# Kernel optimization log

Hardware: AMD Instinct MI355X
Metric: run time of the kernel (lower is better)

Reference implementation:

```python
import jax, jax.numpy as jnp
import numpy as np

D = 1024  # input_size == hidden_size (required by the module's math)
B = 32768

def _linear_params(key, out_dim, in_dim):
    kw, kb = jax.random.split(key)
    bound = 1.0 / np.sqrt(in_dim)
    W = jax.random.uniform(kw, (out_dim, in_dim), jnp.float32, -bound, bound)
    b = jax.random.uniform(kb, (out_dim,), jnp.float32, -bound, bound)
    return W, b

def setup_inputs() -> dict:
    key = jax.random.key(0)
    ks = jax.random.split(key, 8)
    inp = {
        "input": jax.random.normal(ks[0], (B, D), jnp.float32),
        "hidden": jax.random.normal(ks[1], (B, D), jnp.float32),
    }
    names = ["ir", "hr", "iz", "hz", "in_", "hn"]
    for name, k in zip(names, ks[2:]):
        W, b = _linear_params(k, D, D)
        inp[f"W_{name}"] = W
        inp[f"b_{name}"] = b
    return inp

def reference(input, hidden, W_ir, b_ir, W_hr, b_hr, W_iz, b_iz, W_hz, b_hz, W_in_, b_in_, W_hn, b_hn):
    # Fuse the three input-side projections and three hidden-side projections
    # into two GEMMs each mathematically identical to six separate Linears.
    lin = lambda x, W, b: x @ W.T + b
    r_t = jax.nn.sigmoid(lin(input, W_ir, b_ir) + lin(hidden, W_hr, b_hr))
    z_t = jax.nn.sigmoid(lin(input, W_iz, b_iz) + lin(hidden, W_hz, b_hz))
    n_t = jnp.tanh(lin(input, W_in_, b_in_) + r_t * lin(hidden, W_hn, b_hn))
    h_t = (1.0 - z_t) * n_t + z_t * hidden
    return (h_t, h_t)
```

## Files before the change

### kernel.cpp

```cpp
#include <hip/hip_runtime.h>
#include <stdint.h>

#define DD 1024
#define BATCH 32768

typedef unsigned short u16;
typedef __attribute__((ext_vector_type(8))) __bf16 bf16x8;
typedef __attribute__((ext_vector_type(4))) float f32x4;
typedef __attribute__((ext_vector_type(4))) unsigned int u32x4;

__device__ __forceinline__ u16 f2bf(float x) {
  unsigned int u = __builtin_bit_cast(unsigned int, x);
  u = u + 0x7FFFu + ((u >> 16) & 1u);
  return (u16)(u >> 16);
}

__global__ void cvt_all(const float4* __restrict__ in0, const float4* __restrict__ in1,
                        const float4* __restrict__ w0, const float4* __restrict__ w1,
                        const float4* __restrict__ w2, const float4* __restrict__ w3,
                        const float4* __restrict__ w4, const float4* __restrict__ w5,
                        ushort4* __restrict__ o0, ushort4* __restrict__ o1,
                        ushort4* __restrict__ ow) {
  int b = blockIdx.x;
  const float4* s; ushort4* d; int rel;
  if (b < 2048)      { s = in0; d = o0; rel = b; }
  else if (b < 4096) { s = in1; d = o1; rel = b - 2048; }
  else {
    int t = b - 4096; int g = t >> 6; rel = t & 63;
    s = (g == 0) ? w0 : (g == 1) ? w1 : (g == 2) ? w2 : (g == 3) ? w3 : (g == 4) ? w4 : w5;
    d = ow + (size_t)g * 262144;
  }
  int i0 = rel * 4096 + threadIdx.x;
#pragma unroll
  for (int j = 0; j < 16; ++j) {
    int i = i0 + j * 256;
    float4 v = s[i];
    ushort4 o;
    o.x = f2bf(v.x); o.y = f2bf(v.y); o.z = f2bf(v.z); o.w = f2bf(v.w);
    d[i] = o;
  }
}

#define ABUF(b) ((b) * 16384)
#define WBUF(b) (32768 + (b) * 12288)

__device__ __forceinline__ bf16x8 ld8(const u16* p) {
  u32x4 v = *reinterpret_cast<const u32x4*>(p);
  return __builtin_bit_cast(bf16x8, v);
}

__device__ __forceinline__ f32x4 mfma16(bf16x8 a, bf16x8 b, f32x4 c) {
  return __builtin_amdgcn_mfma_f32_16x16x32_bf16(a, b, c, 0, 0, 0);
}

__device__ __forceinline__ void stage_one(const u16* src, const u16* dst) {
  __builtin_amdgcn_global_load_lds(
      (const __attribute__((address_space(1))) void*)src,
      (__attribute__((address_space(3))) void*)dst, 16, 0, 0);
}

__global__ __launch_bounds__(512, 2) void gru_fused(
    const u16* __restrict__ ain, const u16* __restrict__ ah,
    const u16* __restrict__ wall, const float* __restrict__ hidf,
    const float* __restrict__ b_ir, const float* __restrict__ b_hr,
    const float* __restrict__ b_iz, const float* __restrict__ b_hz,
    const float* __restrict__ b_in, const float* __restrict__ b_hn,
    float* __restrict__ out) {
  __shared__ __align__(16) u16 lds[69632];

  int bid = blockIdx.x;
  int x = bid & 7;
  int s = bid >> 3;
  int mb = (x << 4) | (s >> 4);
  int nb = s & 15;

  int tid = threadIdx.x;
  int wid = tid >> 6;
  int lane = tid & 63;
  int r15 = lane & 15;
  int kb = lane >> 4;
  int wm = wid >> 1;
  int wn = wid & 1;

  const f32x4 zero = {0.f, 0.f, 0.f, 0.f};
  f32x4 acc_r[4][2], acc_z[4][2], acc_n[4][2], acc_hn[4][2];
#pragma unroll
  for (int i = 0; i < 4; ++i)
#pragma unroll
    for (int j = 0; j < 2; ++j) {
      acc_r[i][j] = zero; acc_z[i][j] = zero;
      acc_n[i][j] = zero; acc_hn[i][j] = zero;
    }

  int lrow = lane >> 2;
  unsigned koff = (unsigned)((((lane & 3) ^ ((lane >> 3) & 3))) << 3);
  const u16* ain_r = ain + (unsigned)(mb * 256 + lrow) * DD + koff;
  const u16* ah_r  = ah  + (unsigned)(mb * 256 + lrow) * DD + koff;
  const u16* w_r   = wall + (unsigned)(nb * 64 + lrow) * DD + koff;
  int sub = wid & 3;
  int g0 = wid >> 2;
  const u16* wsrc = w_r + (unsigned)(sub * 16) * DD;

  auto stageA = [&](int kt1) {
    unsigned kc = (unsigned)(kt1 << 5);
    int base = ABUF(kt1 & 1);
    stage_one(ain_r + (unsigned)(wid * 16) * DD + kc,       &lds[base + wid * 512]);
    stage_one(ain_r + (unsigned)((wid + 8) * 16) * DD + kc, &lds[base + (wid + 8) * 512]);
    stage_one(ah_r  + (unsigned)(wid * 16) * DD + kc,       &lds[base + 8192 + wid * 512]);
    stage_one(ah_r  + (unsigned)((wid + 8) * 16) * DD + kc, &lds[base + 8192 + (wid + 8) * 512]);
  };
  auto stageW = [&](int kt2, int wb) {
    unsigned kc = (unsigned)(kt2 << 5);
    int base = WBUF(wb);
    stage_one(wsrc + ((unsigned)g0 << 20) + kc,       &lds[base + g0 * 2048 + sub * 512]);
    stage_one(wsrc + ((unsigned)(g0 + 2) << 20) + kc, &lds[base + (g0 + 2) * 2048 + sub * 512]);
    stage_one(wsrc + ((unsigned)(g0 + 4) << 20) + kc, &lds[base + (g0 + 4) * 2048 + sub * 512]);
  };

  int slsw = ((r15 >> 1) & 3);
  int slx = (kb ^ slsw) << 3;

  bf16x8 afi[4], afh[4], bw[6];

  stageA(0); stageW(0, 0); stageA(1); stageW(1, 1);

  int wcur = 0;
  int wnx2 = 2;
  for (int kt = 0; kt < 32; ++kt) {
    if (kt == 0) {
      asm volatile("s_waitcnt vmcnt(7)" ::: "memory");
    } else if (kt == 31) {
      asm volatile("s_waitcnt vmcnt(0)" ::: "memory");
    } else {
      asm volatile("s_waitcnt vmcnt(3)" ::: "memory");
    }
    __builtin_amdgcn_s_barrier();
    __builtin_amdgcn_sched_barrier(0);

    const u16* BA = &lds[ABUF(kt & 1)];
    const u16* BW = &lds[WBUF(wcur)];

#pragma unroll
    for (int i = 0; i < 4; ++i) {
      int Rm = (wm << 6) + (i << 4) + r15;
      afi[i] = ld8(BA + Rm * 32 + slx);
      afh[i] = ld8(BA + 8192 + Rm * 32 + slx);
    }
    {
      int Rn = (wn << 5) + r15;
      const u16* W0 = BW + Rn * 32 + slx;
#pragma unroll
      for (int g = 0; g < 6; ++g) bw[g] = ld8(W0 + g * 2048);
    }
    asm volatile("s_waitcnt lgkmcnt(0)" ::: "memory");
    __builtin_amdgcn_sched_barrier(0);
    if (kt >= 1 && kt < 31) stageA(kt + 1);
    __builtin_amdgcn_s_setprio(1);
#pragma unroll
    for (int i = 0; i < 4; ++i) {
      acc_r[i][0]  = mfma16(afi[i], bw[0], acc_r[i][0]);
      acc_r[i][0]  = mfma16(afh[i], bw[1], acc_r[i][0]);
      acc_z[i][0]  = mfma16(afi[i], bw[2], acc_z[i][0]);
      acc_z[i][0]  = mfma16(afh[i], bw[3], acc_z[i][0]);
      acc_n[i][0]  = mfma16(afi[i], bw[4], acc_n[i][0]);
      acc_hn[i][0] = mfma16(afh[i], bw[5], acc_hn[i][0]);
    }
    __builtin_amdgcn_s_setprio(0);
    __builtin_amdgcn_s_barrier();
    __builtin_amdgcn_sched_barrier(0);

    {
      int Rn = (wn << 5) + 16 + r15;
      const u16* W0 = BW + Rn * 32 + slx;
#pragma unroll
      for (int g = 0; g < 6; ++g) bw[g] = ld8(W0 + g * 2048);
    }
    asm volatile("s_waitcnt lgkmcnt(0)" ::: "memory");
    __builtin_amdgcn_sched_barrier(0);
    if (kt < 30) stageW(kt + 2, wnx2);
    __builtin_amdgcn_s_setprio(1);
#pragma unroll
    for (int i = 0; i < 4; ++i) {
      acc_r[i][1]  = mfma16(afi[i], bw[0], acc_r[i][1]);
      acc_r[i][1]  = mfma16(afh[i], bw[1], acc_r[i][1]);
      acc_z[i][1]  = mfma16(afi[i], bw[2], acc_z[i][1]);
      acc_z[i][1]  = mfma16(afh[i], bw[3], acc_z[i][1]);
      acc_n[i][1]  = mfma16(afi[i], bw[4], acc_n[i][1]);
      acc_hn[i][1] = mfma16(afh[i], bw[5], acc_hn[i][1]);
    }
    __builtin_amdgcn_s_setprio(0);
    wcur = (wcur == 2) ? 0 : wcur + 1;
    wnx2 = (wnx2 == 2) ? 0 : wnx2 + 1;
  }

#pragma unroll
  for (int jf = 0; jf < 2; ++jf) {
    int col = (nb << 6) + (wn << 5) + (jf << 4) + r15;
    float brc = b_ir[col] + b_hr[col];
    float bzc = b_iz[col] + b_hz[col];
    float bnc = b_in[col];
    float bhc = b_hn[col];
#pragma unroll
    for (int i = 0; i < 4; ++i) {
      int row0 = (mb << 8) + (wm << 6) + (i << 4) + (kb << 2);
#pragma unroll
      for (int q = 0; q < 4; ++q) {
        int row = row0 + q;
        float vr = acc_r[i][jf][q] + brc;
        float vz = acc_z[i][jf][q] + bzc;
        float vn = acc_n[i][jf][q] + bnc;
        float vh = acc_hn[i][jf][q] + bhc;
        float rg = __builtin_amdgcn_rcpf(1.f + __expf(-vr));
        float zg = __builtin_amdgcn_rcpf(1.f + __expf(-vz));
        float pre = vn + rg * vh;
        float ax = fabsf(pre);
        float e2 = __expf(-2.f * ax);
        float th = copysignf((1.f - e2) * __builtin_amdgcn_rcpf(1.f + e2), pre);
        float hp = hidf[((size_t)row << 10) + col];
        float h = (1.f - zg) * th + zg * hp;
        size_t o = ((size_t)row << 10) + col;
        out[o] = h;
        out[o + (size_t)BATCH * DD] = h;
      }
    }
  }
}

extern "C" void kernel_launch(void* const* d_in, const int* in_sizes, int n_in,
                              void* d_out, int out_size, void* d_ws, size_t ws_size,
                              hipStream_t stream) {
  (void)in_sizes; (void)n_in; (void)out_size; (void)ws_size;
  const float* inp = (const float*)d_in[0];
  const float* hid = (const float*)d_in[1];
  u16* ws_in  = (u16*)d_ws;
  u16* ws_hid = ws_in + (size_t)BATCH * DD;
  u16* ws_w   = ws_hid + (size_t)BATCH * DD;

  hipLaunchKernelGGL(cvt_all, dim3(4480), dim3(256), 0, stream,
                     (const float4*)inp, (const float4*)hid,
                     (const float4*)d_in[2], (const float4*)d_in[4],
                     (const float4*)d_in[6], (const float4*)d_in[8],
                     (const float4*)d_in[10], (const float4*)d_in[12],
                     (ushort4*)ws_in, (ushort4*)ws_hid, (ushort4*)ws_w);

  hipLaunchKernelGGL(gru_fused, dim3(2048), dim3(512), 0, stream,
                     ws_in, ws_hid, ws_w, hid,
                     (const float*)d_in[3], (const float*)d_in[5],
                     (const float*)d_in[7], (const float*)d_in[9],
                     (const float*)d_in[11], (const float*)d_in[13],
                     (float*)d_out);
}
```

Baseline: 582.3 us.

## Split GEMM main loop into four phases with staggered A staging

The per-k-tile loop now runs four phases instead of two. Each phase loads three W fragments (not six) and then runs a smaller MFMA burst. The A-tile global-to-LDS staging is split into input and hidden halves and issued in different phases, and the prologue no longer prefetches the second A tile. The aim is to interleave LDS reads, global staging and MFMA work more finely and to cut fragment register pressure, at the cost of an extra barrier and lgkmcnt wait per phase.

Result: no change. 577.9 us (-0.8%).

```diff
diff --git a/kernel.cpp b/kernel.cpp
--- a/kernel.cpp
+++ b/kernel.cpp
@@ -101,13 +101,17 @@
   int g0 = wid >> 2;
   const u16* wsrc = w_r + (unsigned)(sub * 16) * DD;
 
-  auto stageA = [&](int kt1) {
+  auto stageAin = [&](int kt1) {
     unsigned kc = (unsigned)(kt1 << 5);
     int base = ABUF(kt1 & 1);
     stage_one(ain_r + (unsigned)(wid * 16) * DD + kc,       &lds[base + wid * 512]);
     stage_one(ain_r + (unsigned)((wid + 8) * 16) * DD + kc, &lds[base + (wid + 8) * 512]);
-    stage_one(ah_r  + (unsigned)(wid * 16) * DD + kc,       &lds[base + 8192 + wid * 512]);
-    stage_one(ah_r  + (unsigned)((wid + 8) * 16) * DD + kc, &lds[base + 8192 + (wid + 8) * 512]);
+  };
+  auto stageAh = [&](int kt1) {
+    unsigned kc = (unsigned)(kt1 << 5);
+    int base = ABUF(kt1 & 1);
+    stage_one(ah_r + (unsigned)(wid * 16) * DD + kc,       &lds[base + 8192 + wid * 512]);
+    stage_one(ah_r + (unsigned)((wid + 8) * 16) * DD + kc, &lds[base + 8192 + (wid + 8) * 512]);
   };
   auto stageW = [&](int kt2, int wb) {
     unsigned kc = (unsigned)(kt2 << 5);
@@ -117,19 +121,16 @@
     stage_one(wsrc + ((unsigned)(g0 + 4) << 20) + kc, &lds[base + (g0 + 4) * 2048 + sub * 512]);
   };
 
-  int slsw = ((r15 >> 1) & 3);
-  int slx = (kb ^ slsw) << 3;
-
-  bf16x8 afi[4], afh[4], bw[6];
-
-  stageA(0); stageW(0, 0); stageA(1); stageW(1, 1);
+  int slx = ((kb ^ ((r15 >> 1) & 3))) << 3;
+
+  bf16x8 afi[4], afh[4], bwA[3], bwB[3];
+
+  stageAin(0); stageAh(0); stageW(0, 0); stageW(1, 1);
 
   int wcur = 0;
   int wnx2 = 2;
   for (int kt = 0; kt < 32; ++kt) {
-    if (kt == 0) {
-      asm volatile("s_waitcnt vmcnt(7)" ::: "memory");
-    } else if (kt == 31) {
+    if (kt == 31) {
       asm volatile("s_waitcnt vmcnt(0)" ::: "memory");
     } else {
       asm volatile("s_waitcnt vmcnt(3)" ::: "memory");
@@ -139,6 +140,8 @@
 
     const u16* BA = &lds[ABUF(kt & 1)];
     const u16* BW = &lds[WBUF(wcur)];
+    const u16* W0 = BW + ((wn << 5) + r15) * 32 + slx;
+    const u16* W1 = BW + ((wn << 5) + 16 + r15) * 32 + slx;
 
 #pragma unroll
     for (int i = 0; i < 4; ++i) {
@@ -146,49 +149,69 @@
       afi[i] = ld8(BA + Rm * 32 + slx);
       afh[i] = ld8(BA + 8192 + Rm * 32 + slx);
     }
-    {
-      int Rn = (wn << 5) + r15;
-      const u16* W0 = BW + Rn * 32 + slx;
-#pragma unroll
-      for (int g = 0; g < 6; ++g) bw[g] = ld8(W0 + g * 2048);
-    }
-    asm volatile("s_waitcnt lgkmcnt(0)" ::: "memory");
-    __builtin_amdgcn_sched_barrier(0);
-    if (kt >= 1 && kt < 31) stageA(kt + 1);
-    __builtin_amdgcn_s_setprio(1);
-#pragma unroll
-    for (int i = 0; i < 4; ++i) {
-      acc_r[i][0]  = mfma16(afi[i], bw[0], acc_r[i][0]);
-      acc_r[i][0]  = mfma16(afh[i], bw[1], acc_r[i][0]);
-      acc_z[i][0]  = mfma16(afi[i], bw[2], acc_z[i][0]);
-      acc_z[i][0]  = mfma16(afh[i], bw[3], acc_z[i][0]);
-      acc_n[i][0]  = mfma16(afi[i], bw[4], acc_n[i][0]);
-      acc_hn[i][0] = mfma16(afh[i], bw[5], acc_hn[i][0]);
-    }
-    __builtin_amdgcn_s_setprio(0);
-    __builtin_amdgcn_s_barrier();
-    __builtin_amdgcn_sched_barrier(0);
-
-    {
-      int Rn = (wn << 5) + 16 + r15;
-      const u16* W0 = BW + Rn * 32 + slx;
-#pragma unroll
-      for (int g = 0; g < 6; ++g) bw[g] = ld8(W0 + g * 2048);
-    }
-    asm volatile("s_waitcnt lgkmcnt(0)" ::: "memory");
-    __builtin_amdgcn_sched_barrier(0);
+    bwA[0] = ld8(W0);
+    bwA[1] = ld8(W0 + 2048);
+    bwA[2] = ld8(W0 + 4096);
+    if (kt < 31) stageAin(kt + 1);
+    __builtin_amdgcn_s_barrier();
+    asm volatile("s_waitcnt lgkmcnt(0)" ::: "memory");
+    __builtin_amdgcn_sched_barrier(0);
+    __builtin_amdgcn_s_setprio(1);
+#pragma unroll
+    for (int i = 0; i < 4; ++i) {
+      acc_r[i][0] = mfma16(afi[i], bwA[0], acc_r[i][0]);
+      acc_r[i][0] = mfma16(afh[i], bwA[1], acc_r[i][0]);
+      acc_z[i][0] = mfma16(afi[i], bwA[2], acc_z[i][0]);
+    }
+    __builtin_amdgcn_s_setprio(0);
+
+    bwB[0] = ld8(W0 + 6144);
+    bwB[1] = ld8(W0 + 8192);
+    bwB[2] = ld8(W0 + 10240);
+    if (kt < 31) stageAh(kt + 1);
+    __builtin_amdgcn_s_barrier();
+    asm volatile("s_waitcnt lgkmcnt(0)" ::: "memory");
+    __builtin_amdgcn_sched_barrier(0);
+    __builtin_amdgcn_s_setprio(1);
+#pragma unroll
+    for (int i = 0; i < 4; ++i) {
+      acc_z[i][0]  = mfma16(afh[i], bwB[0], acc_z[i][0]);
+      acc_n[i][0]  = mfma16(afi[i], bwB[1], acc_n[i][0]);
+      acc_hn[i][0] = mfma16(afh[i], bwB[2], acc_hn[i][0]);
+    }
+    __builtin_amdgcn_s_setprio(0);
+
+    bwA[0] = ld8(W1);
+    bwA[1] = ld8(W1 + 2048);
+    bwA[2] = ld8(W1 + 4096);
     if (kt < 30) stageW(kt + 2, wnx2);
-    __builtin_amdgcn_s_setprio(1);
-#pragma unroll
-    for (int i = 0; i < 4; ++i) {
-      acc_r[i][1]  = mfma16(afi[i], bw[0], acc_r[i][1]);
-      acc_r[i][1]  = mfma16(afh[i], bw[1], acc_r[i][1]);
-      acc_z[i][1]  = mfma16(afi[i], bw[2], acc_z[i][1]);
-      acc_z[i][1]  = mfma16(afh[i], bw[3], acc_z[i][1]);
-      acc_n[i][1]  = mfma16(afi[i], bw[4], acc_n[i][1]);
-      acc_hn[i][1] = mfma16(afh[i], bw[5], acc_hn[i][1]);
-    }
-    __builtin_amdgcn_s_setprio(0);
+    __builtin_amdgcn_s_barrier();
+    asm volatile("s_waitcnt lgkmcnt(0)" ::: "memory");
+    __builtin_amdgcn_sched_barrier(0);
+    __builtin_amdgcn_s_setprio(1);
+#pragma unroll
+    for (int i = 0; i < 4; ++i) {
+      acc_r[i][1] = mfma16(afi[i], bwA[0], acc_r[i][1]);
+      acc_r[i][1] = mfma16(afh[i], bwA[1], acc_r[i][1]);
+      acc_z[i][1] = mfma16(afi[i], bwA[2], acc_z[i][1]);
+    }
+    __builtin_amdgcn_s_setprio(0);
+
+    bwB[0] = ld8(W1 + 6144);
+    bwB[1] = ld8(W1 + 8192);
+    bwB[2] = ld8(W1 + 10240);
+    __builtin_amdgcn_s_barrier();
+    asm volatile("s_waitcnt lgkmcnt(0)" ::: "memory");
+    __builtin_amdgcn_sched_barrier(0);
+    __builtin_amdgcn_s_setprio(1);
+#pragma unroll
+    for (int i = 0; i < 4; ++i) {
+      acc_z[i][1]  = mfma16(afh[i], bwB[0], acc_z[i][1]);
+      acc_n[i][1]  = mfma16(afi[i], bwB[1], acc_n[i][1]);
+      acc_hn[i][1] = mfma16(afh[i], bwB[2], acc_hn[i][1]);
+    }
+    __builtin_amdgcn_s_setprio(0);
+
     wcur = (wcur == 2) ? 0 : wcur + 1;
     wnx2 = (wnx2 == 2) ? 0 : wnx2 + 1;
   }
```
